# Optimization experiments

Measured on AMD Instinct MI355X. Metric: run time of the kernel, lower is better.

The kernel has to match this reference:

```python
import jax, jax.numpy as jnp
import numpy as np

NUM_EXPERTS = 8
TOP_K = 2


def _swiglu(x, w1, w2, w3):
    # x: [T, D], w1/w3: [D, H], w2: [H, D]
    return (jax.nn.silu(x @ w1) * (x @ w3)) @ w2


def setup_inputs() -> dict:
    key = jax.random.key(0)
    ks = jax.random.split(key, 9)
    B, S, D, H, E = 1, 1024, 1024, 1024, NUM_EXPERTS
    std = 0.02
    return {
        "x": jax.random.normal(ks[0], (B, S, D), jnp.float32),
        "router_w": jax.random.normal(ks[1], (D, E), jnp.float32) * std,
        "expert_bias": jnp.zeros((E,), jnp.float32),
        "w1": jax.random.normal(ks[2], (E, D, H), jnp.float32) * std,
        "w2": jax.random.normal(ks[3], (E, H, D), jnp.float32) * std,
        "w3": jax.random.normal(ks[4], (E, D, H), jnp.float32) * std,
        "sw1": jax.random.normal(ks[5], (D, H), jnp.float32) * std,
        "sw2": jax.random.normal(ks[6], (H, D), jnp.float32) * std,
        "sw3": jax.random.normal(ks[7], (D, H), jnp.float32) * std,
    }


def reference(x, router_w, expert_bias, w1, w2, w3, sw1, sw2, sw3):
    B, S, D = x.shape
    E, K = NUM_EXPERTS, TOP_K
    N = B * S
    x_flat = x.reshape(N, D)

    # ---- Router: softmax scores, top-k selection with load-balance bias ----
    logits = x_flat @ router_w                              # [N, E]
    scores = jax.nn.softmax(logits.astype(jnp.float32), axis=-1)
    _, sel = jax.lax.top_k(scores + expert_bias[None, :], K)  # [N, K]
    top_scores = jnp.take_along_axis(scores, sel, axis=-1)    # [N, K] (bias-free weights)

    # ---- Reorder tokens by expert (stable sort) ----
    flat_exp = sel.reshape(-1)                               # [N*K]
    order = jnp.argsort(flat_exp)                            # stable, [T] indices into N*K
    exp_sorted = flat_exp[order]                             # [T]
    routed_input = x_flat[order // K]                        # [T, D]

    # ---- Grouped expert SwiGLU (per-expert masked GEMMs) ----
    routed_output = jnp.zeros_like(routed_input)
    for e in range(E):
        mask = (exp_sorted == e)[:, None]
        y_e = _swiglu(routed_input, w1[e], w2[e], w3[e])
        routed_output = routed_output + jnp.where(mask, y_e, 0.0)

    # ---- Scatter back to unsorted layout and combine with scores ----
    unsorted = jnp.zeros((N * K, D), routed_output.dtype).at[order].set(routed_output)
    unsorted = unsorted.reshape(N, K, D)
    out_experts = jnp.einsum("nk,nkd->nd", top_scores, unsorted)

    # ---- Shared expert ----
    shared_out = _swiglu(x_flat, sw1, sw2, sw3)

    return (shared_out + out_experts).reshape(B, S, D)
```

## Files before the change

### kernel.cpp

```cpp
#include <hip/hip_runtime.h>
#include <hip/hip_bf16.h>

typedef __bf16 bf16_t;
typedef __bf16 bf16x8 __attribute__((ext_vector_type(8)));
typedef float  f32x4  __attribute__((ext_vector_type(4)));
typedef unsigned int u32x4 __attribute__((ext_vector_type(4)));

#define DDIM 1024
#define NTOK 1024
#define MATN (1024 * 1024)
#define BK 64
#define KTILES 4

#define BAR()   asm volatile("s_barrier" ::: "memory")
#define WVM(n)  asm volatile("s_waitcnt vmcnt(" #n ")" ::: "memory")
#define WLG0()  asm volatile("s_waitcnt lgkmcnt(0)" ::: "memory")

__device__ __forceinline__ void load16(const bf16_t* g, bf16_t* l) {
  __builtin_amdgcn_global_load_lds(
      (__attribute__((address_space(1))) void*)(g),
      (__attribute__((address_space(3))) void*)(l), 16, 0, 0);
}

__device__ __forceinline__ int sw_off(int row, int kk) {
  return row * BK + (((kk >> 3) ^ (row & 7)) << 3);
}

__global__ void prep_k(const float* __restrict__ x, bf16_t* __restrict__ xb,
                       float* __restrict__ out, int* __restrict__ list,
                       float* __restrict__ wrow,
                       const float* __restrict__ rw, const float* __restrict__ bias,
                       int* __restrict__ tsel, float* __restrict__ tscore) {
  __shared__ float red[4][8];
  const int tid = threadIdx.x;
  const int i = blockIdx.x * 256 + tid;
  const int j = i * 8;
  const f32x4 a = *(const f32x4*)(x + j);
  const f32x4 b = *(const f32x4*)(x + j + 4);
  bf16x8 v;
#pragma unroll
  for (int t = 0; t < 4; ++t) { v[t] = (bf16_t)a[t]; v[t + 4] = (bf16_t)b[t]; }
  *(bf16x8*)(xb + j) = v;
  const f32x4 z = {0.f, 0.f, 0.f, 0.f};
  *(f32x4*)(out + j) = z; *(f32x4*)(out + j + 4) = z;
  if (i < 4096) { list[i] = 0; wrow[i] = 0.f; }

  const int dbase = (tid & 127) * 8;
  float acc[8];
#pragma unroll
  for (int e = 0; e < 8; ++e) acc[e] = 0.f;
#pragma unroll
  for (int t = 0; t < 8; ++t) {
    const float xv = (t < 4) ? a[t] : b[t - 4];
    const f32x4 w0 = *(const f32x4*)(rw + (dbase + t) * 8);
    const f32x4 w1 = *(const f32x4*)(rw + (dbase + t) * 8 + 4);
#pragma unroll
    for (int e = 0; e < 4; ++e) { acc[e] += xv * w0[e]; acc[e + 4] += xv * w1[e]; }
  }
#pragma unroll
  for (int off = 32; off >= 1; off >>= 1)
#pragma unroll
    for (int e = 0; e < 8; ++e) acc[e] += __shfl_xor(acc[e], off, 64);
  const int lane = tid & 63, wave = tid >> 6;
  if (lane == 0) {
#pragma unroll
    for (int e = 0; e < 8; ++e) red[wave][e] = acc[e];
  }
  __syncthreads();
  if ((tid & 127) == 0) {
    const int n = blockIdx.x * 2 + (tid >> 7);
    float lg[8];
#pragma unroll
    for (int e = 0; e < 8; ++e) lg[e] = red[wave][e] + red[wave + 1][e];
    float mx = lg[0];
#pragma unroll
    for (int e = 1; e < 8; ++e) mx = fmaxf(mx, lg[e]);
    float p[8], s = 0.f;
#pragma unroll
    for (int e = 0; e < 8; ++e) { p[e] = __expf(lg[e] - mx); s += p[e]; }
    const float inv = 1.f / s;
    float sc[8], sb2[8];
#pragma unroll
    for (int e = 0; e < 8; ++e) { sc[e] = p[e] * inv; sb2[e] = sc[e] + bias[e]; }
    int i1 = 0;
#pragma unroll
    for (int e = 1; e < 8; ++e) if (sb2[e] > sb2[i1]) i1 = e;
    int i2 = (i1 == 0) ? 1 : 0;
#pragma unroll
    for (int e = 0; e < 8; ++e) if (e != i2 && e != i1 && sb2[e] > sb2[i2]) i2 = e;
    tsel[n * 2 + 0] = i1; tscore[n * 2 + 0] = sc[i1];
    tsel[n * 2 + 1] = i2; tscore[n * 2 + 1] = sc[i2];
  }
}

__global__ void pack_k(const int* __restrict__ tsel, const float* __restrict__ tscore,
                       int* __restrict__ ntp, int* __restrict__ tile_e,
                       int* __restrict__ tile_m0, int* __restrict__ list,
                       float* __restrict__ wrow) {
  __shared__ int scnt[8];
  __shared__ int sb[9];
  const int tid = threadIdx.x;
  if (tid < 8) scnt[tid] = 0;
  __syncthreads();
  const int e0 = tsel[tid * 2 + 0];
  const int p0 = atomicAdd(&scnt[e0], 1);
  const int e1 = tsel[tid * 2 + 1];
  const int p1 = atomicAdd(&scnt[e1], 1);
  __syncthreads();
  if (tid == 0) {
    int pt = 0, base = 0;
    for (int e = 0; e < 8; ++e) {
      sb[e] = base;
      const int nt = (scnt[e] + 127) >> 7;
      for (int jj = 0; jj < nt; ++jj) { tile_e[pt] = e; tile_m0[pt] = base + jj * 128; ++pt; }
      base += nt << 7;
    }
    sb[8] = base;
    for (int jj = 0; jj < 8; ++jj) { tile_e[pt] = 8; tile_m0[pt] = base + jj * 128; ++pt; }
    ntp[0] = pt;
  }
  __syncthreads();
  const int s0 = sb[e0] + p0; list[s0] = tid; wrow[s0] = tscore[tid * 2 + 0];
  const int s1 = sb[e1] + p1; list[s1] = tid; wrow[s1] = tscore[tid * 2 + 1];
  const int ss = sb[8] + tid; list[ss] = tid; wrow[ss] = 1.f;
}

__global__ void transpose3_k(const float* __restrict__ a8, const float* __restrict__ aS,
                             bf16_t* __restrict__ da,
                             const float* __restrict__ b8, const float* __restrict__ bS,
                             bf16_t* __restrict__ db,
                             const float* __restrict__ c8, const float* __restrict__ cS,
                             bf16_t* __restrict__ dc) {
  const int z = blockIdx.z, kind = z / 9, e = z % 9;
  const float* src;
  bf16_t* dst;
  if (kind == 0)      { src = (e < 8) ? a8 + (size_t)e * MATN : aS; dst = da + (size_t)e * MATN; }
  else if (kind == 1) { src = (e < 8) ? b8 + (size_t)e * MATN : bS; dst = db + (size_t)e * MATN; }
  else                { src = (e < 8) ? c8 + (size_t)e * MATN : cS; dst = dc + (size_t)e * MATN; }

  __shared__ unsigned int T[2][64][33];
  const int t = threadIdx.x;
  const int n0 = blockIdx.x * 64;
  const int kbase = blockIdx.y * (KTILES * 64);
  const int kp = t >> 3, cg = t & 7;
  const int rn = t >> 2, q = t & 3;

  const float* sp = src + (size_t)(2 * kp) * DDIM + n0 + cg * 8;
  bf16_t* dp = dst + (size_t)(n0 + rn) * DDIM + kbase;

  f32x4 a0, a1, b0, b1;
  {
    const float* s0 = sp + (size_t)kbase * DDIM;
    a0 = *(const f32x4*)(s0);        a1 = *(const f32x4*)(s0 + 4);
    b0 = *(const f32x4*)(s0 + DDIM); b1 = *(const f32x4*)(s0 + DDIM + 4);
  }
#pragma unroll
  for (int j = 0; j < KTILES; ++j) {
    const int buf = j & 1;
#pragma unroll
    for (int jj = 0; jj < 4; ++jj) {
      union { bf16_t h[2]; unsigned int u; } p;
      p.h[0] = (bf16_t)a0[jj]; p.h[1] = (bf16_t)b0[jj];
      T[buf][cg * 8 + jj][kp] = p.u;
      p.h[0] = (bf16_t)a1[jj]; p.h[1] = (bf16_t)b1[jj];
      T[buf][cg * 8 + 4 + jj][kp] = p.u;
    }
    if (j < KTILES - 1) {
      const float* s0 = sp + (size_t)(kbase + (j + 1) * 64) * DDIM;
      a0 = *(const f32x4*)(s0);        a1 = *(const f32x4*)(s0 + 4);
      b0 = *(const f32x4*)(s0 + DDIM); b1 = *(const f32x4*)(s0 + DDIM + 4);
    }
    WLG0(); BAR();
    unsigned int r0[4], r1[4];
#pragma unroll
    for (int i = 0; i < 4; ++i) { r0[i] = T[buf][rn][q * 4 + i]; r1[i] = T[buf][rn][q * 4 + 16 + i]; }
    const u32x4 v0 = { r0[0], r0[1], r0[2], r0[3] };
    const u32x4 v1 = { r1[0], r1[1], r1[2], r1[3] };
    bf16_t* d = dp + j * 64;
    *(u32x4*)(d + q * 8) = v0;
    *(u32x4*)(d + q * 8 + 32) = v1;
  }
}

__global__ __launch_bounds__(256, 2)
void gemm12_k(const bf16_t* __restrict__ xb, const bf16_t* __restrict__ wt1,
              const bf16_t* __restrict__ wt3, bf16_t* __restrict__ G,
              const int* __restrict__ tile_e, const int* __restrict__ tile_m0,
              const int* __restrict__ ntp, const int* __restrict__ list) {
  const int ti = blockIdx.y;
  if (ti >= ntp[0]) return;
  const int e = tile_e[ti], slot0 = tile_m0[ti];
  const int n0 = blockIdx.x * 64;

  __shared__ __align__(16) bf16_t sA[2][128 * BK];
  __shared__ __align__(16) bf16_t sB1[2][64 * BK];
  __shared__ __align__(16) bf16_t sB3[2][64 * BK];

  const int lane = threadIdx.x & 63, wave = threadIdx.x >> 6;
  const int wm = wave & 1, wn = wave >> 1;
  const int srr = lane >> 3;
  const int scol = ((lane & 7) ^ srr) * 8;

  const bf16_t *aS[4], *b1S[2], *b3S[2];
#pragma unroll
  for (int i = 0; i < 4; ++i) {
    const int c = wave * 4 + i;
    const int r = c * 8 + srr;
    aS[i] = xb + (size_t)list[slot0 + r] * DDIM + scol;
  }
#pragma unroll
  for (int i = 0; i < 2; ++i) {
    const int c = wave * 2 + i;
    const int r = c * 8 + srr;
    const size_t wb = (size_t)e * MATN + (size_t)(n0 + r) * DDIM + scol;
    b1S[i] = wt1 + wb; b3S[i] = wt3 + wb;
  }

  const f32x4 z = {0.f, 0.f, 0.f, 0.f};
  f32x4 aU[4][2], aV[4][2];
#pragma unroll
  for (int a = 0; a < 4; ++a)
#pragma unroll
    for (int b = 0; b < 2; ++b) { aU[a][b] = z; aV[a][b] = z; }

#define ISSUE12(j, b)                                            \
  _Pragma("unroll") for (int i = 0; i < 4; ++i)                  \
    load16(aS[i] + (j) * BK, &sA[b][(wave * 4 + i) * 512]);      \
  _Pragma("unroll") for (int i = 0; i < 2; ++i) {                \
    load16(b1S[i] + (j) * BK, &sB1[b][(wave * 2 + i) * 512]);    \
    load16(b3S[i] + (j) * BK, &sB3[b][(wave * 2 + i) * 512]);    \
  }

#define COMPUTE12(b)                                                          \
  _Pragma("unroll") for (int ks = 0; ks < 2; ++ks) {                          \
    const int kk = ks * 32 + ((lane >> 4) * 8);                               \
    bf16x8 af[4], f1[2], f3[2];                                               \
    _Pragma("unroll") for (int mf = 0; mf < 4; ++mf)                          \
      af[mf] = *(const bf16x8*)&sA[b][sw_off(wm * 64 + mf * 16 + (lane & 15), kk)]; \
    _Pragma("unroll") for (int nf = 0; nf < 2; ++nf) {                        \
      const int ro = sw_off(wn * 32 + nf * 16 + (lane & 15), kk);             \
      f1[nf] = *(const bf16x8*)&sB1[b][ro];                                   \
      f3[nf] = *(const bf16x8*)&sB3[b][ro];                                   \
    }                                                                         \
    _Pragma("unroll") for (int nf = 0; nf < 2; ++nf)                          \
      _Pragma("unroll") for (int mf = 0; mf < 4; ++mf) {                      \
        aU[mf][nf] = __builtin_amdgcn_mfma_f32_16x16x32_bf16(af[mf], f1[nf], aU[mf][nf], 0, 0, 0); \
        aV[mf][nf] = __builtin_amdgcn_mfma_f32_16x16x32_bf16(af[mf], f3[nf], aV[mf][nf], 0, 0, 0); \
      }                                                                       \
  }

  ISSUE12(0, 0);
#pragma unroll
  for (int j = 0; j < 15; ++j) {
    ISSUE12(j + 1, (j + 1) & 1);
    WVM(8); BAR();
    COMPUTE12(j & 1);
    BAR();
  }
  WVM(0); BAR();
  COMPUTE12(1);

  const int colb = n0 + wn * 32 + (lane & 15);
#pragma unroll
  for (int mf = 0; mf < 4; ++mf)
#pragma unroll
    for (int rg = 0; rg < 4; ++rg) {
      const int row = wm * 64 + mf * 16 + ((lane >> 4) * 4) + rg;
      bf16_t* gp = G + (size_t)(slot0 + row) * DDIM + colb;
#pragma unroll
      for (int nf = 0; nf < 2; ++nf) {
        const float u = aU[mf][nf][rg];
        gp[nf * 16] = (bf16_t)((u / (1.f + __expf(-u))) * aV[mf][nf][rg]);
      }
    }
#undef ISSUE12
#undef COMPUTE12
}

template <int MODE>
__global__ __launch_bounds__(256, 3)
void gemmS_k(const bf16_t* __restrict__ Asrc, const bf16_t* __restrict__ wt,
             bf16_t* __restrict__ UG, float* __restrict__ oacc,
             const int* __restrict__ tile_e, const int* __restrict__ tile_m0,
             const int* __restrict__ ntp, const int* __restrict__ list,
             const float* __restrict__ wrow) {
  const int ti = blockIdx.y;
  if (ti >= ntp[0]) return;
  const int e = tile_e[ti], slot0 = tile_m0[ti];
  const int n0 = blockIdx.x * 64;

  __shared__ __align__(16) bf16_t sA[2][128 * BK];
  __shared__ __align__(16) bf16_t sB[2][64 * BK];

  const int lane = threadIdx.x & 63, wave = threadIdx.x >> 6;
  const int wm = wave & 1, wn = wave >> 1;
  const int srr = lane >> 3;
  const int scol = ((lane & 7) ^ srr) * 8;

  const bf16_t *aS[4], *bS[2];
#pragma unroll
  for (int i = 0; i < 4; ++i) {
    const int c = wave * 4 + i;
    const int r = c * 8 + srr;
    const int slot = slot0 + r;
    aS[i] = Asrc + (size_t)((MODE == 2) ? slot : list[slot]) * DDIM + scol;
  }
#pragma unroll
  for (int i = 0; i < 2; ++i) {
    const int c = wave * 2 + i;
    const int r = c * 8 + srr;
    bS[i] = wt + (size_t)e * MATN + (size_t)(n0 + r) * DDIM + scol;
  }

  const f32x4 z = {0.f, 0.f, 0.f, 0.f};
  f32x4 acc[4][2];
#pragma unroll
  for (int a = 0; a < 4; ++a)
#pragma unroll
    for (int b = 0; b < 2; ++b) acc[a][b] = z;

#define ISSUES(j, b)                                           \
  _Pragma("unroll") for (int i = 0; i < 4; ++i)                \
    load16(aS[i] + (j) * BK, &sA[b][(wave * 4 + i) * 512]);    \
  _Pragma("unroll") for (int i = 0; i < 2; ++i)                \
    load16(bS[i] + (j) * BK, &sB[b][(wave * 2 + i) * 512]);

#define COMPUTES(b)                                                           \
  _Pragma("unroll") for (int ks = 0; ks < 2; ++ks) {                          \
    const int kk = ks * 32 + ((lane >> 4) * 8);                               \
    bf16x8 af[4], fb[2];                                                      \
    _Pragma("unroll") for (int mf = 0; mf < 4; ++mf)                          \
      af[mf] = *(const bf16x8*)&sA[b][sw_off(wm * 64 + mf * 16 + (lane & 15), kk)]; \
    _Pragma("unroll") for (int nf = 0; nf < 2; ++nf)                          \
      fb[nf] = *(const bf16x8*)&sB[b][sw_off(wn * 32 + nf * 16 + (lane & 15), kk)]; \
    _Pragma("unroll") for (int nf = 0; nf < 2; ++nf)                          \
      _Pragma("unroll") for (int mf = 0; mf < 4; ++mf)                        \
        acc[mf][nf] = __builtin_amdgcn_mfma_f32_16x16x32_bf16(af[mf], fb[nf], acc[mf][nf], 0, 0, 0); \
  }

  ISSUES(0, 0);
#pragma unroll
  for (int j = 0; j < 15; ++j) {
    ISSUES(j + 1, (j + 1) & 1);
    WVM(6); BAR();
    COMPUTES(j & 1);
    BAR();
  }
  WVM(0); BAR();
  COMPUTES(1);

  const int colb = n0 + wn * 32 + (lane & 15);
#pragma unroll
  for (int mf = 0; mf < 4; ++mf)
#pragma unroll
    for (int rg = 0; rg < 4; ++rg) {
      const int row = wm * 64 + mf * 16 + ((lane >> 4) * 4) + rg;
      const int slot = slot0 + row;
      if (MODE == 0) {
        bf16_t* gp = UG + (size_t)slot * DDIM + colb;
#pragma unroll
        for (int nf = 0; nf < 2; ++nf) gp[nf * 16] = (bf16_t)acc[mf][nf][rg];
      } else if (MODE == 1) {
        bf16_t* gp = UG + (size_t)slot * DDIM + colb;
#pragma unroll
        for (int nf = 0; nf < 2; ++nf) {
          const float u = (float)gp[nf * 16];
          gp[nf * 16] = (bf16_t)((u / (1.f + __expf(-u))) * acc[mf][nf][rg]);
        }
      } else {
        const float w = wrow[slot];
        if (w != 0.f) {
          float* dst = oacc + (size_t)list[slot] * DDIM + colb;
#pragma unroll
          for (int nf = 0; nf < 2; ++nf)
            atomicAdd(dst + nf * 16, w * acc[mf][nf][rg]);
        }
      }
    }
#undef ISSUES
#undef COMPUTES
}

extern "C" void kernel_launch(void* const* d_in, const int* in_sizes, int n_in,
                              void* d_out, int out_size, void* d_ws, size_t ws_size,
                              hipStream_t stream) {
  (void)in_sizes; (void)n_in; (void)out_size;
  const float* x   = (const float*)d_in[0];
  const float* rw  = (const float*)d_in[1];
  const float* eb  = (const float*)d_in[2];
  const float* w1  = (const float*)d_in[3];
  const float* w2  = (const float*)d_in[4];
  const float* w3  = (const float*)d_in[5];
  const float* sw1 = (const float*)d_in[6];
  const float* sw2 = (const float*)d_in[7];
  const float* sw3 = (const float*)d_in[8];
  float* out = (float*)d_out;

  char* ws = (char*)d_ws;
  const size_t WT  = 18874368;
  const size_t XBS = 2097152, GS = 8388608, MS = 65536;
  const int mode = (ws_size >= 3 * WT + XBS + GS + MS) ? 3
                 : (ws_size >= 2 * WT + XBS + GS + MS) ? 2 : 1;

  size_t off = 0;
  bf16_t* wtA = (bf16_t*)(ws); off += WT;
  bf16_t* wtB = wtA; bf16_t* wtC = wtA;
  if (mode >= 2) { wtB = (bf16_t*)(ws + off); off += WT; }
  if (mode == 3) { wtC = (bf16_t*)(ws + off); off += WT; }
  bf16_t* xb = (bf16_t*)(ws + off); off += XBS;
  bf16_t* G  = (bf16_t*)(ws + off); off += GS;
  int* meta  = (int*)(ws + off);

  int*   ntp     = meta + 32;
  int*   tile_e  = meta + 40;
  int*   tile_m0 = meta + 104;
  int*   tsel    = meta + 168;
  int*   list    = meta + 4264;
  float* tscore  = (float*)(meta + 8360);
  float* wrow    = (float*)(meta + 10408);

  const int YT = 1024 / 64 / KTILES;

  prep_k<<<512, 256, 0, stream>>>(x, xb, out, list, wrow, rw, eb, tsel, tscore);
  pack_k<<<1, 1024, 0, stream>>>(tsel, tscore, ntp, tile_e, tile_m0, list, wrow);

  if (mode == 3) {
    transpose3_k<<<dim3(16, YT, 27), 256, 0, stream>>>(w1, sw1, wtA, w3, sw3, wtB, w2, sw2, wtC);
    gemm12_k<<<dim3(16, 31), 256, 0, stream>>>(xb, wtA, wtB, G, tile_e, tile_m0, ntp, list);
    gemmS_k<2><<<dim3(16, 31), 256, 0, stream>>>(G, wtC, G, out, tile_e, tile_m0, ntp, list, wrow);
  } else if (mode == 2) {
    transpose3_k<<<dim3(16, YT, 18), 256, 0, stream>>>(w1, sw1, wtA, w3, sw3, wtB, w3, sw3, wtB);
    gemm12_k<<<dim3(16, 31), 256, 0, stream>>>(xb, wtA, wtB, G, tile_e, tile_m0, ntp, list);
    transpose3_k<<<dim3(16, YT, 9), 256, 0, stream>>>(w2, sw2, wtA, w2, sw2, wtA, w2, sw2, wtA);
    gemmS_k<2><<<dim3(16, 31), 256, 0, stream>>>(G, wtA, G, out, tile_e, tile_m0, ntp, list, wrow);
  } else {
    transpose3_k<<<dim3(16, YT, 9), 256, 0, stream>>>(w1, sw1, wtA, w1, sw1, wtA, w1, sw1, wtA);
    gemmS_k<0><<<dim3(16, 31), 256, 0, stream>>>(xb, wtA, G, out, tile_e, tile_m0, ntp, list, wrow);
    transpose3_k<<<dim3(16, YT, 9), 256, 0, stream>>>(w3, sw3, wtA, w3, sw3, wtA, w3, sw3, wtA);
    gemmS_k<1><<<dim3(16, 31), 256, 0, stream>>>(xb, wtA, G, out, tile_e, tile_m0, ntp, list, wrow);
    transpose3_k<<<dim3(16, YT, 9), 256, 0, stream>>>(w2, sw2, wtA, w2, sw2, wtA, w2, sw2, wtA);
    gemmS_k<2><<<dim3(16, 31), 256, 0, stream>>>(G, wtA, G, out, tile_e, tile_m0, ntp, list, wrow);
  }
}
```

Measured before the change: 211.6 us.

## Shrink GEMM tiles to 64x64 with BK 32 and fuse prep into transpose kernel

The GEMM kernels drop from 128-row to 64-row M tiles with a 32-wide K step. Expert groups are padded to 64 instead of 128, which cuts wasted padded rows, raises the grid to 56 tile rows, and lets occupancy rise to 4 blocks per CU. The router/prep kernel is merged into the weight transpose launch as extra z-slices, which removes one launch and lets the two run concurrently. In exchange, each LDS tile is reused less, there are twice as many K iterations with barriers, and the swizzle pattern changes.

```diff
diff --git a/kernel.cpp b/kernel.cpp
--- a/kernel.cpp
+++ b/kernel.cpp
@@ -9,7 +9,7 @@
 #define DDIM 1024
 #define NTOK 1024
 #define MATN (1024 * 1024)
-#define BK 64
+#define BK 32
 #define KTILES 4
 
 #define BAR()   asm volatile("s_barrier" ::: "memory")
@@ -23,73 +23,134 @@
 }
 
 __device__ __forceinline__ int sw_off(int row, int kk) {
-  return row * BK + (((kk >> 3) ^ (row & 7)) << 3);
-}
-
-__global__ void prep_k(const float* __restrict__ x, bf16_t* __restrict__ xb,
-                       float* __restrict__ out, int* __restrict__ list,
-                       float* __restrict__ wrow,
-                       const float* __restrict__ rw, const float* __restrict__ bias,
-                       int* __restrict__ tsel, float* __restrict__ tscore) {
-  __shared__ float red[4][8];
+  const int h = (row & 3) ^ ((row >> 2) & 3);
+  return row * BK + (((kk >> 3) ^ h) << 3);
+}
+
+__global__ void fused_pt_k(const float* __restrict__ a8, const float* __restrict__ aS,
+                           bf16_t* __restrict__ da,
+                           const float* __restrict__ b8, const float* __restrict__ bS,
+                           bf16_t* __restrict__ db,
+                           const float* __restrict__ c8, const float* __restrict__ cS,
+                           bf16_t* __restrict__ dc, int nzt,
+                           const float* __restrict__ x, bf16_t* __restrict__ xb,
+                           float* __restrict__ out, int* __restrict__ list,
+                           float* __restrict__ wrow,
+                           const float* __restrict__ rw, const float* __restrict__ bias,
+                           int* __restrict__ tsel, float* __restrict__ tscore) {
+  __shared__ unsigned int T[2][64][33];
   const int tid = threadIdx.x;
-  const int i = blockIdx.x * 256 + tid;
-  const int j = i * 8;
-  const f32x4 a = *(const f32x4*)(x + j);
-  const f32x4 b = *(const f32x4*)(x + j + 4);
-  bf16x8 v;
-#pragma unroll
-  for (int t = 0; t < 4; ++t) { v[t] = (bf16_t)a[t]; v[t + 4] = (bf16_t)b[t]; }
-  *(bf16x8*)(xb + j) = v;
-  const f32x4 z = {0.f, 0.f, 0.f, 0.f};
-  *(f32x4*)(out + j) = z; *(f32x4*)(out + j + 4) = z;
-  if (i < 4096) { list[i] = 0; wrow[i] = 0.f; }
-
-  const int dbase = (tid & 127) * 8;
-  float acc[8];
-#pragma unroll
-  for (int e = 0; e < 8; ++e) acc[e] = 0.f;
-#pragma unroll
-  for (int t = 0; t < 8; ++t) {
-    const float xv = (t < 4) ? a[t] : b[t - 4];
-    const f32x4 w0 = *(const f32x4*)(rw + (dbase + t) * 8);
-    const f32x4 w1 = *(const f32x4*)(rw + (dbase + t) * 8 + 4);
-#pragma unroll
-    for (int e = 0; e < 4; ++e) { acc[e] += xv * w0[e]; acc[e + 4] += xv * w1[e]; }
-  }
-#pragma unroll
-  for (int off = 32; off >= 1; off >>= 1)
-#pragma unroll
-    for (int e = 0; e < 8; ++e) acc[e] += __shfl_xor(acc[e], off, 64);
-  const int lane = tid & 63, wave = tid >> 6;
-  if (lane == 0) {
-#pragma unroll
-    for (int e = 0; e < 8; ++e) red[wave][e] = acc[e];
-  }
-  __syncthreads();
-  if ((tid & 127) == 0) {
-    const int n = blockIdx.x * 2 + (tid >> 7);
-    float lg[8];
-#pragma unroll
-    for (int e = 0; e < 8; ++e) lg[e] = red[wave][e] + red[wave + 1][e];
-    float mx = lg[0];
-#pragma unroll
-    for (int e = 1; e < 8; ++e) mx = fmaxf(mx, lg[e]);
-    float p[8], s = 0.f;
-#pragma unroll
-    for (int e = 0; e < 8; ++e) { p[e] = __expf(lg[e] - mx); s += p[e]; }
-    const float inv = 1.f / s;
-    float sc[8], sb2[8];
-#pragma unroll
-    for (int e = 0; e < 8; ++e) { sc[e] = p[e] * inv; sb2[e] = sc[e] + bias[e]; }
-    int i1 = 0;
-#pragma unroll
-    for (int e = 1; e < 8; ++e) if (sb2[e] > sb2[i1]) i1 = e;
-    int i2 = (i1 == 0) ? 1 : 0;
-#pragma unroll
-    for (int e = 0; e < 8; ++e) if (e != i2 && e != i1 && sb2[e] > sb2[i2]) i2 = e;
-    tsel[n * 2 + 0] = i1; tscore[n * 2 + 0] = sc[i1];
-    tsel[n * 2 + 1] = i2; tscore[n * 2 + 1] = sc[i2];
+
+  if ((int)blockIdx.z >= nzt) {
+    float (*red)[8] = (float (*)[8])&T[0][0][0];
+    const int pid = (blockIdx.z - nzt) * 64 + blockIdx.y * 16 + blockIdx.x;
+    const int i = pid * 256 + tid;
+    const int j = i * 8;
+    const f32x4 a = *(const f32x4*)(x + j);
+    const f32x4 b = *(const f32x4*)(x + j + 4);
+    bf16x8 v;
+#pragma unroll
+    for (int t = 0; t < 4; ++t) { v[t] = (bf16_t)a[t]; v[t + 4] = (bf16_t)b[t]; }
+    *(bf16x8*)(xb + j) = v;
+    const f32x4 z = {0.f, 0.f, 0.f, 0.f};
+    *(f32x4*)(out + j) = z; *(f32x4*)(out + j + 4) = z;
+    if (i < 4096) { list[i] = 0; wrow[i] = 0.f; }
+
+    const int dbase = (tid & 127) * 8;
+    float acc[8];
+#pragma unroll
+    for (int e = 0; e < 8; ++e) acc[e] = 0.f;
+#pragma unroll
+    for (int t = 0; t < 8; ++t) {
+      const float xv = (t < 4) ? a[t] : b[t - 4];
+      const f32x4 w0 = *(const f32x4*)(rw + (dbase + t) * 8);
+      const f32x4 w1 = *(const f32x4*)(rw + (dbase + t) * 8 + 4);
+#pragma unroll
+      for (int e = 0; e < 4; ++e) { acc[e] += xv * w0[e]; acc[e + 4] += xv * w1[e]; }
+    }
+#pragma unroll
+    for (int off = 32; off >= 1; off >>= 1)
+#pragma unroll
+      for (int e = 0; e < 8; ++e) acc[e] += __shfl_xor(acc[e], off, 64);
+    const int lane = tid & 63, wave = tid >> 6;
+    if (lane == 0) {
+#pragma unroll
+      for (int e = 0; e < 8; ++e) red[wave][e] = acc[e];
+    }
+    __syncthreads();
+    if ((tid & 127) == 0) {
+      const int n = pid * 2 + (tid >> 7);
+      float lg[8];
+#pragma unroll
+      for (int e = 0; e < 8; ++e) lg[e] = red[wave][e] + red[wave + 1][e];
+      float mx = lg[0];
+#pragma unroll
+      for (int e = 1; e < 8; ++e) mx = fmaxf(mx, lg[e]);
+      float p[8], s = 0.f;
+#pragma unroll
+      for (int e = 0; e < 8; ++e) { p[e] = __expf(lg[e] - mx); s += p[e]; }
+      const float inv = 1.f / s;
+      float sc[8], sb2[8];
+#pragma unroll
+      for (int e = 0; e < 8; ++e) { sc[e] = p[e] * inv; sb2[e] = sc[e] + bias[e]; }
+      int i1 = 0;
+#pragma unroll
+      for (int e = 1; e < 8; ++e) if (sb2[e] > sb2[i1]) i1 = e;
+      int i2 = (i1 == 0) ? 1 : 0;
+#pragma unroll
+      for (int e = 0; e < 8; ++e) if (e != i2 && e != i1 && sb2[e] > sb2[i2]) i2 = e;
+      tsel[n * 2 + 0] = i1; tscore[n * 2 + 0] = sc[i1];
+      tsel[n * 2 + 1] = i2; tscore[n * 2 + 1] = sc[i2];
+    }
+    return;
+  }
+
+  const int z = blockIdx.z, kind = z / 9, e = z % 9;
+  const float* src;
+  bf16_t* dst;
+  if (kind == 0)      { src = (e < 8) ? a8 + (size_t)e * MATN : aS; dst = da + (size_t)e * MATN; }
+  else if (kind == 1) { src = (e < 8) ? b8 + (size_t)e * MATN : bS; dst = db + (size_t)e * MATN; }
+  else                { src = (e < 8) ? c8 + (size_t)e * MATN : cS; dst = dc + (size_t)e * MATN; }
+
+  const int n0 = blockIdx.x * 64;
+  const int kbase = blockIdx.y * (KTILES * 64);
+  const int kp = tid >> 3, cg = tid & 7;
+  const int rn = tid >> 2, q = tid & 3;
+
+  const float* sp = src + (size_t)(2 * kp) * DDIM + n0 + cg * 8;
+  bf16_t* dp = dst + (size_t)(n0 + rn) * DDIM + kbase;
+
+  f32x4 a0, a1, b0, b1;
+  {
+    const float* s0 = sp + (size_t)kbase * DDIM;
+    a0 = *(const f32x4*)(s0);        a1 = *(const f32x4*)(s0 + 4);
+    b0 = *(const f32x4*)(s0 + DDIM); b1 = *(const f32x4*)(s0 + DDIM + 4);
+  }
+#pragma unroll
+  for (int j = 0; j < KTILES; ++j) {
+    const int buf = j & 1;
+#pragma unroll
+    for (int jj = 0; jj < 4; ++jj) {
+      union { bf16_t h[2]; unsigned int u; } p;
+      p.h[0] = (bf16_t)a0[jj]; p.h[1] = (bf16_t)b0[jj];
+      T[buf][cg * 8 + jj][kp] = p.u;
+      p.h[0] = (bf16_t)a1[jj]; p.h[1] = (bf16_t)b1[jj];
+      T[buf][cg * 8 + 4 + jj][kp] = p.u;
+    }
+    if (j < KTILES - 1) {
+      const float* s0 = sp + (size_t)(kbase + (j + 1) * 64) * DDIM;
+      a0 = *(const f32x4*)(s0);        a1 = *(const f32x4*)(s0 + 4);
+      b0 = *(const f32x4*)(s0 + DDIM); b1 = *(const f32x4*)(s0 + DDIM + 4);
+    }
+    WLG0(); BAR();
+    unsigned int r0[4], r1[4];
+#pragma unroll
+    for (int i = 0; i < 4; ++i) { r0[i] = T[buf][rn][q * 4 + i]; r1[i] = T[buf][rn][q * 4 + 16 + i]; }
+    const u32x4 v0 = { r0[0], r0[1], r0[2], r0[3] };
+    const u32x4 v1 = { r1[0], r1[1], r1[2], r1[3] };
+    bf16_t* d = dp + j * 64;
+    *(u32x4*)(d + q * 8) = v0;
+    *(u32x4*)(d + q * 8 + 32) = v1;
   }
 }
 
@@ -111,12 +172,12 @@
     int pt = 0, base = 0;
     for (int e = 0; e < 8; ++e) {
       sb[e] = base;
-      const int nt = (scnt[e] + 127) >> 7;
-      for (int jj = 0; jj < nt; ++jj) { tile_e[pt] = e; tile_m0[pt] = base + jj * 128; ++pt; }
-      base += nt << 7;
+      const int nt = (scnt[e] + 63) >> 6;
+      for (int jj = 0; jj < nt; ++jj) { tile_e[pt] = e; tile_m0[pt] = base + jj * 64; ++pt; }
+      base += nt << 6;
     }
     sb[8] = base;
-    for (int jj = 0; jj < 8; ++jj) { tile_e[pt] = 8; tile_m0[pt] = base + jj * 128; ++pt; }
+    for (int jj = 0; jj < 16; ++jj) { tile_e[pt] = 8; tile_m0[pt] = base + jj * 64; ++pt; }
     ntp[0] = pt;
   }
   __syncthreads();
@@ -125,64 +186,7 @@
   const int ss = sb[8] + tid; list[ss] = tid; wrow[ss] = 1.f;
 }
 
-__global__ void transpose3_k(const float* __restrict__ a8, const float* __restrict__ aS,
-                             bf16_t* __restrict__ da,
-                             const float* __restrict__ b8, const float* __restrict__ bS,
-                             bf16_t* __restrict__ db,
-                             const float* __restrict__ c8, const float* __restrict__ cS,
-                             bf16_t* __restrict__ dc) {
-  const int z = blockIdx.z, kind = z / 9, e = z % 9;
-  const float* src;
-  bf16_t* dst;
-  if (kind == 0)      { src = (e < 8) ? a8 + (size_t)e * MATN : aS; dst = da + (size_t)e * MATN; }
-  else if (kind == 1) { src = (e < 8) ? b8 + (size_t)e * MATN : bS; dst = db + (size_t)e * MATN; }
-  else                { src = (e < 8) ? c8 + (size_t)e * MATN : cS; dst = dc + (size_t)e * MATN; }
-
-  __shared__ unsigned int T[2][64][33];
-  const int t = threadIdx.x;
-  const int n0 = blockIdx.x * 64;
-  const int kbase = blockIdx.y * (KTILES * 64);
-  const int kp = t >> 3, cg = t & 7;
-  const int rn = t >> 2, q = t & 3;
-
-  const float* sp = src + (size_t)(2 * kp) * DDIM + n0 + cg * 8;
-  bf16_t* dp = dst + (size_t)(n0 + rn) * DDIM + kbase;
-
-  f32x4 a0, a1, b0, b1;
-  {
-    const float* s0 = sp + (size_t)kbase * DDIM;
-    a0 = *(const f32x4*)(s0);        a1 = *(const f32x4*)(s0 + 4);
-    b0 = *(const f32x4*)(s0 + DDIM); b1 = *(const f32x4*)(s0 + DDIM + 4);
-  }
-#pragma unroll
-  for (int j = 0; j < KTILES; ++j) {
-    const int buf = j & 1;
-#pragma unroll
-    for (int jj = 0; jj < 4; ++jj) {
-      union { bf16_t h[2]; unsigned int u; } p;
-      p.h[0] = (bf16_t)a0[jj]; p.h[1] = (bf16_t)b0[jj];
-      T[buf][cg * 8 + jj][kp] = p.u;
-      p.h[0] = (bf16_t)a1[jj]; p.h[1] = (bf16_t)b1[jj];
-      T[buf][cg * 8 + 4 + jj][kp] = p.u;
-    }
-    if (j < KTILES - 1) {
-      const float* s0 = sp + (size_t)(kbase + (j + 1) * 64) * DDIM;
-      a0 = *(const f32x4*)(s0);        a1 = *(const f32x4*)(s0 + 4);
-      b0 = *(const f32x4*)(s0 + DDIM); b1 = *(const f32x4*)(s0 + DDIM + 4);
-    }
-    WLG0(); BAR();
-    unsigned int r0[4], r1[4];
-#pragma unroll
-    for (int i = 0; i < 4; ++i) { r0[i] = T[buf][rn][q * 4 + i]; r1[i] = T[buf][rn][q * 4 + 16 + i]; }
-    const u32x4 v0 = { r0[0], r0[1], r0[2], r0[3] };
-    const u32x4 v1 = { r1[0], r1[1], r1[2], r1[3] };
-    bf16_t* d = dp + j * 64;
-    *(u32x4*)(d + q * 8) = v0;
-    *(u32x4*)(d + q * 8 + 32) = v1;
-  }
-}
-
-__global__ __launch_bounds__(256, 2)
+__global__ __launch_bounds__(256, 4)
 void gemm12_k(const bf16_t* __restrict__ xb, const bf16_t* __restrict__ wt1,
               const bf16_t* __restrict__ wt3, bf16_t* __restrict__ G,
               const int* __restrict__ tile_e, const int* __restrict__ tile_m0,
@@ -192,58 +196,47 @@
   const int e = tile_e[ti], slot0 = tile_m0[ti];
   const int n0 = blockIdx.x * 64;
 
-  __shared__ __align__(16) bf16_t sA[2][128 * BK];
+  __shared__ __align__(16) bf16_t sA[2][64 * BK];
   __shared__ __align__(16) bf16_t sB1[2][64 * BK];
   __shared__ __align__(16) bf16_t sB3[2][64 * BK];
 
   const int lane = threadIdx.x & 63, wave = threadIdx.x >> 6;
   const int wm = wave & 1, wn = wave >> 1;
-  const int srr = lane >> 3;
-  const int scol = ((lane & 7) ^ srr) * 8;
-
-  const bf16_t *aS[4], *b1S[2], *b3S[2];
-#pragma unroll
-  for (int i = 0; i < 4; ++i) {
-    const int c = wave * 4 + i;
-    const int r = c * 8 + srr;
-    aS[i] = xb + (size_t)list[slot0 + r] * DDIM + scol;
-  }
-#pragma unroll
-  for (int i = 0; i < 2; ++i) {
-    const int c = wave * 2 + i;
-    const int r = c * 8 + srr;
-    const size_t wb = (size_t)e * MATN + (size_t)(n0 + r) * DDIM + scol;
-    b1S[i] = wt1 + wb; b3S[i] = wt3 + wb;
+  const int srow = wave * 16 + (lane >> 2);
+  const int scol = (((lane & 3) ^ ((lane >> 2) & 3) ^ ((lane >> 4) & 3)) << 3);
+
+  const bf16_t *aS, *b1S, *b3S;
+  aS = xb + (size_t)list[slot0 + srow] * DDIM + scol;
+  {
+    const size_t wb = (size_t)e * MATN + (size_t)(n0 + srow) * DDIM + scol;
+    b1S = wt1 + wb; b3S = wt3 + wb;
   }
 
   const f32x4 z = {0.f, 0.f, 0.f, 0.f};
-  f32x4 aU[4][2], aV[4][2];
-#pragma unroll
-  for (int a = 0; a < 4; ++a)
+  f32x4 aU[2][2], aV[2][2];
+#pragma unroll
+  for (int a = 0; a < 2; ++a)
 #pragma unroll
     for (int b = 0; b < 2; ++b) { aU[a][b] = z; aV[a][b] = z; }
 
-#define ISSUE12(j, b)                                            \
-  _Pragma("unroll") for (int i = 0; i < 4; ++i)                  \
-    load16(aS[i] + (j) * BK, &sA[b][(wave * 4 + i) * 512]);      \
-  _Pragma("unroll") for (int i = 0; i < 2; ++i) {                \
-    load16(b1S[i] + (j) * BK, &sB1[b][(wave * 2 + i) * 512]);    \
-    load16(b3S[i] + (j) * BK, &sB3[b][(wave * 2 + i) * 512]);    \
-  }
+#define ISSUE12(j, b)                          \
+  load16(aS  + (j) * BK, &sA[b][wave * 512]);  \
+  load16(b1S + (j) * BK, &sB1[b][wave * 512]); \
+  load16(b3S + (j) * BK, &sB3[b][wave * 512]);
 
 #define COMPUTE12(b)                                                          \
-  _Pragma("unroll") for (int ks = 0; ks < 2; ++ks) {                          \
-    const int kk = ks * 32 + ((lane >> 4) * 8);                               \
-    bf16x8 af[4], f1[2], f3[2];                                               \
-    _Pragma("unroll") for (int mf = 0; mf < 4; ++mf)                          \
-      af[mf] = *(const bf16x8*)&sA[b][sw_off(wm * 64 + mf * 16 + (lane & 15), kk)]; \
+  {                                                                           \
+    const int kk = (lane >> 4) * 8;                                           \
+    bf16x8 af[2], f1[2], f3[2];                                               \
+    _Pragma("unroll") for (int mf = 0; mf < 2; ++mf)                          \
+      af[mf] = *(const bf16x8*)&sA[b][sw_off(wm * 32 + mf * 16 + (lane & 15), kk)]; \
     _Pragma("unroll") for (int nf = 0; nf < 2; ++nf) {                        \
       const int ro = sw_off(wn * 32 + nf * 16 + (lane & 15), kk);             \
       f1[nf] = *(const bf16x8*)&sB1[b][ro];                                   \
       f3[nf] = *(const bf16x8*)&sB3[b][ro];                                   \
     }                                                                         \
     _Pragma("unroll") for (int nf = 0; nf < 2; ++nf)                          \
-      _Pragma("unroll") for (int mf = 0; mf < 4; ++mf) {                      \
+      _Pragma("unroll") for (int mf = 0; mf < 2; ++mf) {                      \
         aU[mf][nf] = __builtin_amdgcn_mfma_f32_16x16x32_bf16(af[mf], f1[nf], aU[mf][nf], 0, 0, 0); \
         aV[mf][nf] = __builtin_amdgcn_mfma_f32_16x16x32_bf16(af[mf], f3[nf], aV[mf][nf], 0, 0, 0); \
       }                                                                       \
@@ -251,9 +244,9 @@
 
   ISSUE12(0, 0);
 #pragma unroll
-  for (int j = 0; j < 15; ++j) {
+  for (int j = 0; j < 31; ++j) {
     ISSUE12(j + 1, (j + 1) & 1);
-    WVM(8); BAR();
+    WVM(3); BAR();
     COMPUTE12(j & 1);
     BAR();
   }
@@ -262,10 +255,10 @@
 
   const int colb = n0 + wn * 32 + (lane & 15);
 #pragma unroll
-  for (int mf = 0; mf < 4; ++mf)
+  for (int mf = 0; mf < 2; ++mf)
 #pragma unroll
     for (int rg = 0; rg < 4; ++rg) {
-      const int row = wm * 64 + mf * 16 + ((lane >> 4) * 4) + rg;
+      const int row = wm * 32 + mf * 16 + ((lane >> 4) * 4) + rg;
       bf16_t* gp = G + (size_t)(slot0 + row) * DDIM + colb;
 #pragma unroll
       for (int nf = 0; nf < 2; ++nf) {
@@ -278,7 +271,7 @@
 }
 
 template <int MODE>
-__global__ __launch_bounds__(256, 3)
+__global__ __launch_bounds__(256, 4)
 void gemmS_k(const bf16_t* __restrict__ Asrc, const bf16_t* __restrict__ wt,
              bf16_t* __restrict__ UG, float* __restrict__ oacc,
              const int* __restrict__ tile_e, const int* __restrict__ tile_m0,
@@ -289,60 +282,47 @@
   const int e = tile_e[ti], slot0 = tile_m0[ti];
   const int n0 = blockIdx.x * 64;
 
-  __shared__ __align__(16) bf16_t sA[2][128 * BK];
+  __shared__ __align__(16) bf16_t sA[2][64 * BK];
   __shared__ __align__(16) bf16_t sB[2][64 * BK];
 
   const int lane = threadIdx.x & 63, wave = threadIdx.x >> 6;
   const int wm = wave & 1, wn = wave >> 1;
-  const int srr = lane >> 3;
-  const int scol = ((lane & 7) ^ srr) * 8;
-
-  const bf16_t *aS[4], *bS[2];
-#pragma unroll
-  for (int i = 0; i < 4; ++i) {
-    const int c = wave * 4 + i;
-    const int r = c * 8 + srr;
-    const int slot = slot0 + r;
-    aS[i] = Asrc + (size_t)((MODE == 2) ? slot : list[slot]) * DDIM + scol;
-  }
-#pragma unroll
-  for (int i = 0; i < 2; ++i) {
-    const int c = wave * 2 + i;
-    const int r = c * 8 + srr;
-    bS[i] = wt + (size_t)e * MATN + (size_t)(n0 + r) * DDIM + scol;
-  }
+  const int srow = wave * 16 + (lane >> 2);
+  const int scol = (((lane & 3) ^ ((lane >> 2) & 3) ^ ((lane >> 4) & 3)) << 3);
+
+  const int slot = slot0 + srow;
+  const bf16_t* aS = Asrc + (size_t)((MODE == 2) ? slot : list[slot]) * DDIM + scol;
+  const bf16_t* bS = wt + (size_t)e * MATN + (size_t)(n0 + srow) * DDIM + scol;
 
   const f32x4 z = {0.f, 0.f, 0.f, 0.f};
-  f32x4 acc[4][2];
-#pragma unroll
-  for (int a = 0; a < 4; ++a)
+  f32x4 acc[2][2];
+#pragma unroll
+  for (int a = 0; a < 2; ++a)
 #pragma unroll
     for (int b = 0; b < 2; ++b) acc[a][b] = z;
 
-#define ISSUES(j, b)                                           \
-  _Pragma("unroll") for (int i = 0; i < 4; ++i)                \
-    load16(aS[i] + (j) * BK, &sA[b][(wave * 4 + i) * 512]);    \
-  _Pragma("unroll") for (int i = 0; i < 2; ++i)                \
-    load16(bS[i] + (j) * BK, &sB[b][(wave * 2 + i) * 512]);
+#define ISSUES(j, b)                          \
+  load16(aS + (j) * BK, &sA[b][wave * 512]);  \
+  load16(bS + (j) * BK, &sB[b][wave * 512]);
 
 #define COMPUTES(b)                                                           \
-  _Pragma("unroll") for (int ks = 0; ks < 2; ++ks) {                          \
-    const int kk = ks * 32 + ((lane >> 4) * 8);                               \
-    bf16x8 af[4], fb[2];                                                      \
-    _Pragma("unroll") for (int mf = 0; mf < 4; ++mf)                          \
-      af[mf] = *(const bf16x8*)&sA[b][sw_off(wm * 64 + mf * 16 + (lane & 15), kk)]; \
+  {                                                                           \
+    const int kk = (lane >> 4) * 8;                                           \
+    bf16x8 af[2], fb[2];                                                      \
+    _Pragma("unroll") for (int mf = 0; mf < 2; ++mf)                          \
+      af[mf] = *(const bf16x8*)&sA[b][sw_off(wm * 32 + mf * 16 + (lane & 15), kk)]; \
     _Pragma("unroll") for (int nf = 0; nf < 2; ++nf)                          \
       fb[nf] = *(const bf16x8*)&sB[b][sw_off(wn * 32 + nf * 16 + (lane & 15), kk)]; \
     _Pragma("unroll") for (int nf = 0; nf < 2; ++nf)                          \
-      _Pragma("unroll") for (int mf = 0; mf < 4; ++mf)                        \
+      _Pragma("unroll") for (int mf = 0; mf < 2; ++mf)                        \
         acc[mf][nf] = __builtin_amdgcn_mfma_f32_16x16x32_bf16(af[mf], fb[nf], acc[mf][nf], 0, 0, 0); \
   }
 
   ISSUES(0, 0);
 #pragma unroll
-  for (int j = 0; j < 15; ++j) {
+  for (int j = 0; j < 31; ++j) {
     ISSUES(j + 1, (j + 1) & 1);
-    WVM(6); BAR();
+    WVM(2); BAR();
     COMPUTES(j & 1);
     BAR();
   }
@@ -351,26 +331,26 @@
 
   const int colb = n0 + wn * 32 + (lane & 15);
 #pragma unroll
-  for (int mf = 0; mf < 4; ++mf)
+  for (int mf = 0; mf < 2; ++mf)
 #pragma unroll
     for (int rg = 0; rg < 4; ++rg) {
-      const int row = wm * 64 + mf * 16 + ((lane >> 4) * 4) + rg;
-      const int slot = slot0 + row;
+      const int row = wm * 32 + mf * 16 + ((lane >> 4) * 4) + rg;
+      const int sl = slot0 + row;
       if (MODE == 0) {
-        bf16_t* gp = UG + (size_t)slot * DDIM + colb;
+        bf16_t* gp = UG + (size_t)sl * DDIM + colb;
 #pragma unroll
         for (int nf = 0; nf < 2; ++nf) gp[nf * 16] = (bf16_t)acc[mf][nf][rg];
       } else if (MODE == 1) {
-        bf16_t* gp = UG + (size_t)slot * DDIM + colb;
+        bf16_t* gp = UG + (size_t)sl * DDIM + colb;
 #pragma unroll
         for (int nf = 0; nf < 2; ++nf) {
           const float u = (float)gp[nf * 16];
           gp[nf * 16] = (bf16_t)((u / (1.f + __expf(-u))) * acc[mf][nf][rg]);
         }
       } else {
-        const float w = wrow[slot];
+        const float w = wrow[sl];
         if (w != 0.f) {
-          float* dst = oacc + (size_t)list[slot] * DDIM + colb;
+          float* dst = oacc + (size_t)list[sl] * DDIM + colb;
 #pragma unroll
           for (int nf = 0; nf < 2; ++nf)
             atomicAdd(dst + nf * 16, w * acc[mf][nf][rg]);
@@ -421,24 +401,36 @@
 
   const int YT = 1024 / 64 / KTILES;
 
-  prep_k<<<512, 256, 0, stream>>>(x, xb, out, list, wrow, rw, eb, tsel, tscore);
-  pack_k<<<1, 1024, 0, stream>>>(tsel, tscore, ntp, tile_e, tile_m0, list, wrow);
-
   if (mode == 3) {
-    transpose3_k<<<dim3(16, YT, 27), 256, 0, stream>>>(w1, sw1, wtA, w3, sw3, wtB, w2, sw2, wtC);
-    gemm12_k<<<dim3(16, 31), 256, 0, stream>>>(xb, wtA, wtB, G, tile_e, tile_m0, ntp, list);
-    gemmS_k<2><<<dim3(16, 31), 256, 0, stream>>>(G, wtC, G, out, tile_e, tile_m0, ntp, list, wrow);
+    fused_pt_k<<<dim3(16, YT, 27 + 8), 256, 0, stream>>>(
+        w1, sw1, wtA, w3, sw3, wtB, w2, sw2, wtC, 27,
+        x, xb, out, list, wrow, rw, eb, tsel, tscore);
+    pack_k<<<1, 1024, 0, stream>>>(tsel, tscore, ntp, tile_e, tile_m0, list, wrow);
+    gemm12_k<<<dim3(16, 56), 256, 0, stream>>>(xb, wtA, wtB, G, tile_e, tile_m0, ntp, list);
+    gemmS_k<2><<<dim3(16, 56), 256, 0, stream>>>(G, wtC, G, out, tile_e, tile_m0, ntp, list, wrow);
   } else if (mode == 2) {
-    transpose3_k<<<dim3(16, YT, 18), 256, 0, stream>>>(w1, sw1, wtA, w3, sw3, wtB, w3, sw3, wtB);
-    gemm12_k<<<dim3(16, 31), 256, 0, stream>>>(xb, wtA, wtB, G, tile_e, tile_m0, ntp, list);
-    transpose3_k<<<dim3(16, YT, 9), 256, 0, stream>>>(w2, sw2, wtA, w2, sw2, wtA, w2, sw2, wtA);
-    gemmS_k<2><<<dim3(16, 31), 256, 0, stream>>>(G, wtA, G, out, tile_e, tile_m0, ntp, list, wrow);
+    fused_pt_k<<<dim3(16, YT, 18 + 8), 256, 0, stream>>>(
+        w1, sw1, wtA, w3, sw3, wtB, w3, sw3, wtB, 18,
+        x, xb, out, list, wrow, rw, eb, tsel, tscore);
+    pack_k<<<1, 1024, 0, stream>>>(tsel, tscore, ntp, tile_e, tile_m0, list, wrow);
+    gemm12_k<<<dim3(16, 56), 256, 0, stream>>>(xb, wtA, wtB, G, tile_e, tile_m0, ntp, list);
+    fused_pt_k<<<dim3(16, YT, 9), 256, 0, stream>>>(
+        w2, sw2, wtA, w2, sw2, wtA, w2, sw2, wtA, 9,
+        x, xb, out, list, wrow, rw, eb, tsel, tscore);
+    gemmS_k<2><<<dim3(16, 56), 256, 0, stream>>>(G, wtA, G, out, tile_e, tile_m0, ntp, list, wrow);
   } else {
-    transpose3_k<<<dim3(16, YT, 9), 256, 0, stream>>>(w1, sw1, wtA, w1, sw1, wtA, w1, sw1, wtA);
-    gemmS_k<0><<<dim3(16, 31), 256, 0, stream>>>(xb, wtA, G, out, tile_e, tile_m0, ntp, list, wrow);
-    transpose3_k<<<dim3(16, YT, 9), 256, 0, stream>>>(w3, sw3, wtA, w3, sw3, wtA, w3, sw3, wtA);
-    gemmS_k<1><<<dim3(16, 31), 256, 0, stream>>>(xb, wtA, G, out, tile_e, tile_m0, ntp, list, wrow);
-    transpose3_k<<<dim3(16, YT, 9), 256, 0, stream>>>(w2, sw2, wtA, w2, sw2, wtA, w2, sw2, wtA);
-    gemmS_k<2><<<dim3(16, 31), 256, 0, stream>>>(G, wtA, G, out, tile_e, tile_m0, ntp, list, wrow);
-  }
-}
+    fused_pt_k<<<dim3(16, YT, 9 + 8), 256, 0, stream>>>(
+        w1, sw1, wtA, w1, sw1, wtA, w1, sw1, wtA, 9,
+        x, xb, out, list, wrow, rw, eb, tsel, tscore);
+    pack_k<<<1, 1024, 0, stream>>>(tsel, tscore, ntp, tile_e, tile_m0, list, wrow);
+    gemmS_k<0><<<dim3(16, 56), 256, 0, stream>>>(xb, wtA, G, out, tile_e, tile_m0, ntp, list, wrow);
+    fused_pt_k<<<dim3(16, YT, 9), 256, 0, stream>>>(
+        w3, sw3, wtA, w3, sw3, wtA, w3, sw3, wtA, 9,
+        x, xb, out, list, wrow, rw, eb, tsel, tscore);
+    gemmS_k<1><<<dim3(16, 56), 256, 0, stream>>>(xb, wtA, G, out, tile_e, tile_m0, ntp, list, wrow);
+    fused_pt_k<<<dim3(16, YT, 9), 256, 0, stream>>>(
+        w2, sw2, wtA, w2, sw2, wtA, w2, sw2, wtA, 9,
+        x, xb, out, list, wrow, rw, eb, tsel, tscore);
+    gemmS_k<2><<<dim3(16, 56), 256, 0, stream>>>(G, wtA, G, out, tile_e, tile_m0, ntp, list, wrow);
+  }
+}
```

Result: slower. 218.2 us (+3.1%).
